# Optimization experiments

Measured on AMD Instinct MI355X. Metric: run time of the kernel, lower is better.

## Reference

```python
import jax, jax.numpy as jnp
import numpy as np

EPS = 1.1920929e-07  # torch RMSNorm default eps = finfo(float32).eps


def segsum(a):
    # a: (..., T) -> (..., T, T); [i, j] = sum_{j < t <= i} a[t] for j <= i, -inf above diag
    T = a.shape[-1]
    cs = jnp.cumsum(a, axis=-1)
    diff = cs[..., :, None] - cs[..., None, :]
    mask = jnp.tril(jnp.ones((T, T), dtype=bool))
    return jnp.where(mask, diff, -jnp.inf)


def dw_causal_conv(x, w):
    # x: (B, L, C), w: (C, K) depthwise causal conv (left pad K-1), matches Conv1d(pad=K-1)[:, :L]
    K = w.shape[-1]
    L = x.shape[1]
    xp = jnp.pad(x, ((0, 0), (K - 1, 0), (0, 0)))
    out = jnp.zeros_like(x)
    for j in range(K):
        out = out + xp[:, j:j + L, :] * w[:, j]
    return out


def ssd(X, A, Bv, Cv, block_len, init_state):
    # X: (B,L,H,P) pre-multiplied by dt; A: (B,L,H) = A*dt; Bv/Cv: (B,L,H,N)
    Bsz, L, H, P = X.shape
    N = Bv.shape[-1]
    c = L // block_len
    Xb = X.reshape(Bsz, c, block_len, H, P)
    Bb = Bv.reshape(Bsz, c, block_len, H, N)
    Cb = Cv.reshape(Bsz, c, block_len, H, N)
    Ab = A.reshape(Bsz, c, block_len, H).transpose(0, 3, 1, 2)  # (B,H,c,l)
    A_cumsum = jnp.cumsum(Ab, axis=-1)
    Ltri = jnp.exp(segsum(Ab))  # (B,H,c,l,l)
    # intra-chunk (diagonal block) output
    Y_diag = jnp.einsum('bclhn,bcshn,bhcls,bcshp->bclhp', Cb, Bb, Ltri, Xb)
    # per-chunk final states
    decay_states = jnp.exp(A_cumsum[..., -1:] - A_cumsum)  # (B,H,c,l)
    states = jnp.einsum('bclhn,bhcl,bclhp->bchpn', Bb, decay_states, Xb)
    states = jnp.concatenate([init_state[:, None], states], axis=1)  # (B,c+1,H,P,N)
    # inter-chunk recurrence via segsum over chunk boundaries
    last_A = A_cumsum[..., -1]  # (B,H,c)
    decay_chunk = jnp.exp(segsum(jnp.pad(last_A, ((0, 0), (0, 0), (1, 0)))))  # (B,H,c+1,c+1)
    new_states = jnp.einsum('bhzc,bchpn->bzhpn', decay_chunk, states)
    states, final_state = new_states[:, :-1], new_states[:, -1]
    # off-diagonal contribution from carried-in states
    state_decay_out = jnp.exp(A_cumsum)  # (B,H,c,l)
    Y_off = jnp.einsum('bclhn,bchpn,bhcl->bclhp', Cb, states, state_decay_out)
    Y = (Y_diag + Y_off).reshape(Bsz, L, H, P)
    return Y, final_state


def setup_inputs():
    key = jax.random.key(0)
    ks = jax.random.split(key, 8)
    d_model, d_state, d_conv, expand, headdim, ngroups = 1024, 128, 4, 2, 64, 1
    d_inner = expand * d_model                      # 2048
    H = d_inner // headdim                          # 32
    proj_out = 2 * d_inner + 2 * ngroups * d_state + H  # 4384
    conv_dim = d_inner + 2 * ngroups * d_state      # 2304
    B, L = 2, 2048
    x = jax.random.normal(ks[0], (B, L, d_model), dtype=jnp.float32)
    state = jnp.zeros((B, H, headdim, d_state), dtype=jnp.float32)
    in_proj_w = jax.random.normal(ks[1], (proj_out, d_model), dtype=jnp.float32) * 0.02
    conv_w = jax.random.normal(ks[2], (conv_dim, d_conv), dtype=jnp.float32) * 0.2
    A_log = jnp.log(jax.random.uniform(ks[3], (H,), minval=1.0, maxval=16.0))
    dt0 = jnp.exp(jax.random.uniform(ks[4], (H,)) * (np.log(0.1) - np.log(0.001)) + np.log(0.001))
    dt0 = jnp.maximum(dt0, 0.0001)
    dt_bias = dt0 + jnp.log(-jnp.expm1(-dt0))
    D_param = jnp.ones((H,), dtype=jnp.float32)
    norm_w = jnp.ones((d_inner,), dtype=jnp.float32)
    out_proj_w = jax.random.normal(ks[5], (d_model, d_inner), dtype=jnp.float32) * 0.02
    return dict(x=x, state=state, in_proj_w=in_proj_w, conv_w=conv_w, A_log=A_log,
                dt_bias=dt_bias, D_param=D_param, norm_w=norm_w, out_proj_w=out_proj_w,
                block_len=64)


def reference(x, state, in_proj_w, conv_w, A_log, dt_bias, D_param, norm_w, out_proj_w, block_len):
    B, L, Dm = x.shape
    H = A_log.shape[0]
    P = state.shape[2]
    N = state.shape[3]
    d_inner = H * P
    conv_dim = conv_w.shape[0]
    zxbcdt = x @ in_proj_w.T  # (B,L,proj_out)
    z = zxbcdt[..., :d_inner]
    xBC = zxbcdt[..., d_inner:d_inner + conv_dim]
    dt = zxbcdt[..., d_inner + conv_dim:]
    xBC = jax.nn.silu(dw_causal_conv(xBC, conv_w))
    x_branch = xBC[..., :d_inner]
    Bv = xBC[..., d_inner:d_inner + N]           # ngroups = 1
    Cv = xBC[..., d_inner + N:]
    X = jax.nn.silu(x_branch.reshape(B, L, H, P))
    Bv = jnp.broadcast_to(jax.nn.silu(Bv)[:, :, None, :], (B, L, H, N))
    Cv = jnp.broadcast_to(jax.nn.silu(Cv)[:, :, None, :], (B, L, H, N))
    A = -jnp.exp(A_log)
    dt = jax.nn.softplus(dt + dt_bias)           # (B,L,H)
    A_dt = A * dt
    X_dt = X * dt[..., None]
    Y, final_state = ssd(X_dt, A_dt, Bv, Cv, block_len, state)
    Y = Y + D_param[None, None, :, None] * X
    y_flat = Y.reshape(B, L, d_inner)
    y_norm = y_flat * jax.lax.rsqrt(jnp.mean(y_flat * y_flat, axis=-1, keepdims=True) + EPS) * norm_w
    y_core = y_norm * jax.nn.sigmoid(z)
    y = y_core @ out_proj_w.T + x
    return (y, final_state)
```

## Files before the change

### kernel.cpp

```cpp
#include <hip/hip_runtime.h>
#include <math.h>

#define BATCH 2
#define LSEQ  2048
#define TTOK  4096
#define DM    1024
#define DI    2048
#define NH    32
#define HP    64
#define NS    128
#define CONVD 2304
#define PROJ  4384
#define NCH   32
#define BLK   64

typedef __bf16 bf16x8 __attribute__((ext_vector_type(8)));
typedef float  f32x4  __attribute__((ext_vector_type(4)));
typedef unsigned short ushortx8 __attribute__((ext_vector_type(8)));
typedef unsigned short ushort_t;
typedef __attribute__((address_space(3))) void  lds_void;
typedef __attribute__((address_space(1))) const void glb_cvoid;

__device__ __forceinline__ float silu_(float x) { return x / (1.f + __expf(-x)); }

__device__ __forceinline__ unsigned short f2bf(float x) {
    union { float f; unsigned u; } u; u.f = x;
    unsigned r = u.u + 0x7fffu + ((u.u >> 16) & 1u);
    return (unsigned short)(r >> 16);
}
__device__ __forceinline__ float bf2f(unsigned short s) {
    union { unsigned u; float f; } u; u.u = ((unsigned)s) << 16; return u.f;
}

__global__ __launch_bounds__(256)
void cast_all_k(const float* __restrict__ x, const float* __restrict__ ipw,
                const float* __restrict__ opw,
                ushort_t* __restrict__ xb, ushort_t* __restrict__ ipb,
                ushort_t* __restrict__ opb)
{
    const int n1 = TTOK*DM, n2 = PROJ*DM;
    int i = (blockIdx.x * 256 + threadIdx.x) * 8;
    const float* src; ushort_t* dst;
    if (i < n1)            { src = x   + i;             dst = xb  + i; }
    else if (i < n1 + n2)  { src = ipw + (i - n1);      dst = ipb + (i - n1); }
    else                   { src = opw + (i - n1 - n2); dst = opb + (i - n1 - n2); }
    float4 a = *(const float4*)(src);
    float4 b = *(const float4*)(src + 4);
    ushortx8 r;
    r[0]=f2bf(a.x); r[1]=f2bf(a.y); r[2]=f2bf(a.z); r[3]=f2bf(a.w);
    r[4]=f2bf(b.x); r[5]=f2bf(b.y); r[6]=f2bf(b.z); r[7]=f2bf(b.w);
    *(ushortx8*)dst = r;
}

template<int TM, int TN, int HASRES, int OUTBF>
__global__ __launch_bounds__(256)
void hgemm_nt(const ushort_t* __restrict__ A, const ushort_t* __restrict__ Bw,
              void* __restrict__ Cp, const float* __restrict__ R,
              int M, int N, int K)
{
    constexpr int MT = TM / 32, NT = TN / 32;
    constexpr int JA = TM / 64, JB = TN / 64;
    __shared__ ushort_t S[(TM + TN) * 64];
    ushort_t* As = S;
    ushort_t* Bs = S + TM * 64;
    char* As_c = (char*)As;
    char* Bs_c = (char*)Bs;
    const int t = threadIdx.x;
    const int l = t & 63, w = t >> 6;

    const int tx_ = (N + TN - 1) / TN, ty_ = (M + TM - 1) / TM;
    int bid = blockIdx.x;
    int sc = bid / (8 * ty_), rem = bid % (8 * ty_);
    int sw_w = min(8, tx_ - sc * 8);
    int bx = sc * 8 + rem % sw_w;
    int by = rem / sw_w;
    const int bm = by * TM, bn = bx * TN;
    const int wm = (w >> 1) * (TM / 2), wn = (w & 1) * (TN / 2);

    const int rowt = t >> 2;
    const int kkt  = (t & 3) * 8;
    const ushort_t* srcA = A + (size_t)(bm + rowt) * K + kkt;
    const ushort_t* srcB[JB];
#pragma unroll
    for (int j = 0; j < JB; ++j) {
        int gr = min(bn + j * 64 + rowt, N - 1);
        srcB[j] = Bw + (size_t)gr * K + kkt;
    }

    f32x4 acc[MT][NT] = {};
    const int fr = l & 15, sel8 = (l >> 4) * 8;

    for (int k0 = 0; k0 < K; k0 += 64) {
        __syncthreads();
#pragma unroll
        for (int h = 0; h < 2; ++h) {
#pragma unroll
            for (int j = 0; j < JA; ++j)
                __builtin_amdgcn_global_load_lds((glb_cvoid*)(srcA + (size_t)j * 64 * K + k0 + h * 32),
                                                 (lds_void*)(As_c + h * TM * 64 + j * 4096 + 16 * t), 16, 0, 0);
#pragma unroll
            for (int j = 0; j < JB; ++j)
                __builtin_amdgcn_global_load_lds((glb_cvoid*)(srcB[j] + k0 + h * 32),
                                                 (lds_void*)(Bs_c + h * TN * 64 + j * 4096 + 16 * t), 16, 0, 0);
        }
        __syncthreads();
#pragma unroll
        for (int h = 0; h < 2; ++h) {
            bf16x8 af[MT], bfr[NT];
#pragma unroll
            for (int mt = 0; mt < MT; ++mt)
                af[mt] = *(const bf16x8*)(As + h * TM * 32 + (wm + mt * 16 + fr) * 32 + sel8);
#pragma unroll
            for (int nt = 0; nt < NT; ++nt)
                bfr[nt] = *(const bf16x8*)(Bs + h * TN * 32 + (wn + nt * 16 + fr) * 32 + sel8);
#pragma unroll
            for (int mt = 0; mt < MT; ++mt)
#pragma unroll
                for (int nt = 0; nt < NT; ++nt)
                    acc[mt][nt] = __builtin_amdgcn_mfma_f32_16x16x32_bf16(af[mt], bfr[nt], acc[mt][nt], 0, 0, 0);
        }
    }

    const int crow = (l >> 4) * 4, ccol = l & 15;
#pragma unroll
    for (int mt = 0; mt < MT; ++mt) {
#pragma unroll
        for (int nt = 0; nt < NT; ++nt) {
            int n = bn + wn + nt * 16 + ccol;
            if (n >= N) continue;
#pragma unroll
            for (int i = 0; i < 4; ++i) {
                int m = bm + wm + mt * 16 + crow + i;
                float v = acc[mt][nt][i];
                if (HASRES) v += R[(size_t)m * N + n];
                if (OUTBF) ((ushort_t*)Cp)[(size_t)m * N + n] = f2bf(v);
                else       ((float*)Cp)[(size_t)m * N + n] = v;
            }
        }
    }
}

#define NCONVB 9216
__global__ __launch_bounds__(256)
void mid1_k(const ushort_t* __restrict__ zx, const float* __restrict__ cw,
            const float* __restrict__ dt_bias, const float* __restrict__ A_log,
            ushort_t* __restrict__ xBC, float* __restrict__ dt_sp, float* __restrict__ cumA)
{
    if (blockIdx.x < NCONVB) {
        int idx = blockIdx.x * 256 + threadIdx.x;
        int c4 = (idx % (CONVD/4)) * 4;
        int tkk = idx / (CONVD/4);
        int b = tkk >> 11, l = tkk & 2047;
        const ushort_t* col = zx + (size_t)b * LSEQ * PROJ + DI + c4;
        float4 w0 = *(const float4*)(cw + c4*4);
        float4 w1 = *(const float4*)(cw + c4*4 + 4);
        float4 w2 = *(const float4*)(cw + c4*4 + 8);
        float4 w3 = *(const float4*)(cw + c4*4 + 12);
        ushort4 tp = *(const ushort4*)(col + (size_t)l * PROJ);
        float a0 = w0.w * bf2f(tp.x), a1 = w1.w * bf2f(tp.y), a2 = w2.w * bf2f(tp.z), a3 = w3.w * bf2f(tp.w);
        if (l >= 1) { ushort4 v = *(const ushort4*)(col + (size_t)(l-1) * PROJ);
            a0 += w0.z*bf2f(v.x); a1 += w1.z*bf2f(v.y); a2 += w2.z*bf2f(v.z); a3 += w3.z*bf2f(v.w); }
        if (l >= 2) { ushort4 v = *(const ushort4*)(col + (size_t)(l-2) * PROJ);
            a0 += w0.y*bf2f(v.x); a1 += w1.y*bf2f(v.y); a2 += w2.y*bf2f(v.z); a3 += w3.y*bf2f(v.w); }
        if (l >= 3) { ushort4 v = *(const ushort4*)(col + (size_t)(l-3) * PROJ);
            a0 += w0.x*bf2f(v.x); a1 += w1.x*bf2f(v.y); a2 += w2.x*bf2f(v.z); a3 += w3.x*bf2f(v.w); }
        ushort4 o;
        o.x = f2bf(silu_(silu_(a0))); o.y = f2bf(silu_(silu_(a1)));
        o.z = f2bf(silu_(silu_(a2))); o.w = f2bf(silu_(silu_(a3)));
        *(ushort4*)(xBC + (size_t)tkk * CONVD + c4) = o;
    } else {
        int wid = (blockIdx.x - NCONVB) * 4 + (threadIdx.x >> 6);
        int ln = threadIdx.x & 63;
        int c = wid & 31, h = (wid >> 5) & 31, b = wid >> 10;
        int tk = b * LSEQ + c * BLK + ln;
        float xv = bf2f(zx[(size_t)tk * PROJ + (DI + CONVD) + h]) + dt_bias[h];
        float dtv = (xv > 20.f) ? xv : log1pf(__expf(xv));
        dt_sp[tk * NH + h] = dtv;
        float val = -__expf(A_log[h]) * dtv;
#pragma unroll
        for (int off = 1; off < 64; off <<= 1) {
            float u = __shfl_up(val, off, 64);
            if (ln >= off) val += u;
        }
        cumA[(size_t)wid * 64 + ln] = val;
    }
}

__global__ __launch_bounds__(256)
void mid2_k(const ushort_t* __restrict__ xBC, const float* __restrict__ dt_sp,
            const float* __restrict__ cumA, float* __restrict__ CBT,
            ushort_t* __restrict__ states)
{
    __shared__ __align__(16) char smem[33408];
    int t = threadIdx.x, r = t >> 2, q = t & 3;
    if (blockIdx.x < 64) {
        int b = blockIdx.x >> 5, c = blockIdx.x & 31;
        float (*sB)[65] = (float(*)[65])smem;
        float (*sC)[65] = sB + 64;
        const ushort_t* xb = xBC + (size_t)(b * LSEQ + c * BLK) * CONVD;
        float acc[16];
#pragma unroll
        for (int i = 0; i < 16; ++i) acc[i] = 0.f;
        for (int half = 0; half < 2; ++half) {
            __syncthreads();
#pragma unroll
            for (int jj = 0; jj < 4; ++jj) {
                ushort4 bv = *(const ushort4*)(xb + (size_t)r * CONVD + DI      + half*64 + q*16 + jj*4);
                ushort4 cv = *(const ushort4*)(xb + (size_t)r * CONVD + DI + NS + half*64 + q*16 + jj*4);
                int col = q*16 + jj*4;
                sB[r][col]=bf2f(bv.x); sB[r][col+1]=bf2f(bv.y); sB[r][col+2]=bf2f(bv.z); sB[r][col+3]=bf2f(bv.w);
                sC[r][col]=bf2f(cv.x); sC[r][col+1]=bf2f(cv.y); sC[r][col+2]=bf2f(cv.z); sC[r][col+3]=bf2f(cv.w);
            }
            __syncthreads();
            for (int n = 0; n < 64; ++n) {
                float cv = sC[r][n];
#pragma unroll
                for (int si = 0; si < 16; ++si)
                    acc[si] += cv * sB[q*16 + si][n];
            }
        }
        float* o = CBT + (size_t)blockIdx.x * 4096 + r * 64 + q * 16;
#pragma unroll
        for (int si = 0; si < 16; ++si) o[si] = acc[si];
    } else {
        int bi = blockIdx.x - 64;
        int h = bi & 31, c = (bi >> 5) & 31, b = bi >> 10;
        ushort_t* XdT = (ushort_t*)smem;
        ushort_t* BdT = XdT + 64 * 72;
        const float* cA = cumA + (size_t)((b*NH + h)*NCH + c) * 64;
        float scale = dt_sp[(b * LSEQ + c * BLK + r) * NH + h] * __expf(cA[63] - cA[r]);
        const ushort_t* xb = xBC + (size_t)(b * LSEQ + c * BLK + r) * CONVD;
#pragma unroll
        for (int jj = 0; jj < 4; ++jj) {
            ushort4 v = *(const ushort4*)(xb + h*HP + q*16 + jj*4);
            int p0 = q*16 + jj*4;
            XdT[(p0+0)*72 + r] = v.x; XdT[(p0+1)*72 + r] = v.y;
            XdT[(p0+2)*72 + r] = v.z; XdT[(p0+3)*72 + r] = v.w;
        }
#pragma unroll
        for (int jj = 0; jj < 8; ++jj) {
            ushort4 v = *(const ushort4*)(xb + DI + q*32 + jj*4);
            int n0 = q*32 + jj*4;
            BdT[(n0+0)*72 + r] = f2bf(bf2f(v.x)*scale);
            BdT[(n0+1)*72 + r] = f2bf(bf2f(v.y)*scale);
            BdT[(n0+2)*72 + r] = f2bf(bf2f(v.z)*scale);
            BdT[(n0+3)*72 + r] = f2bf(bf2f(v.w)*scale);
        }
        __syncthreads();
        int ln = t & 63, w = t >> 6;
        int wm = (w >> 1) * 32, wn = (w & 1) * 64;
        int fr = ln & 15;
        f32x4 acc[2][4] = {};
#pragma unroll
        for (int ks = 0; ks < 2; ++ks) {
            int koff = ks*32 + (ln >> 4) * 8;
            bf16x8 af[2], bv[4];
#pragma unroll
            for (int mt = 0; mt < 2; ++mt) af[mt] = *(const bf16x8*)&XdT[(wm + mt*16 + fr)*72 + koff];
#pragma unroll
            for (int nt = 0; nt < 4; ++nt) bv[nt] = *(const bf16x8*)&BdT[(wn + nt*16 + fr)*72 + koff];
#pragma unroll
            for (int mt = 0; mt < 2; ++mt)
#pragma unroll
                for (int nt = 0; nt < 4; ++nt)
                    acc[mt][nt] = __builtin_amdgcn_mfma_f32_16x16x32_bf16(af[mt], bv[nt], acc[mt][nt], 0, 0, 0);
        }
        ushort_t* o = states + (size_t)((b*NCH + c)*NH + h) * 8192;
        int crow = (ln >> 4) * 4, ccol = ln & 15;
#pragma unroll
        for (int mt = 0; mt < 2; ++mt)
#pragma unroll
            for (int nt = 0; nt < 4; ++nt)
#pragma unroll
                for (int i = 0; i < 4; ++i)
                    o[(wm + mt*16 + crow + i)*128 + wn + nt*16 + ccol] = f2bf(acc[mt][nt][i]);
    }
}

__global__ __launch_bounds__(256)
void scan_k(const float* __restrict__ init_state, const float* __restrict__ cumA,
            const ushort_t* __restrict__ states, ushort_t* __restrict__ pref,
            float* __restrict__ out_final)
{
    int idx = blockIdx.x * 256 + threadIdx.x;
    int h = (idx >> 13) & 31, b = idx >> 18;
    int pn = idx & 8191;
    float run = init_state[idx];
    const float* cAb = cumA + (size_t)(b*NH + h) * NCH * 64;
    for (int c = 0; c < NCH; ++c) {
        float la = cAb[c*64 + 63];
        size_t off = (size_t)((b*NCH + c)*NH + h) * 8192 + pn;
        float tmp = bf2f(states[off]);
        pref[off] = f2bf(run);
        run = expf(la) * run + tmp;
    }
    out_final[idx] = run;
}

__global__ __launch_bounds__(256)
void y_mfma_k(const ushort_t* __restrict__ xBC, const float* __restrict__ dt_sp,
              const float* __restrict__ cumA, const float* __restrict__ CBT,
              const ushort_t* __restrict__ pref, const float* __restrict__ D_param,
              ushort_t* __restrict__ Y)
{
    int bi = blockIdx.x;
    int h = bi & 31, c = (bi >> 5) & 31, b = bi >> 10;
    __shared__ ushort_t Wm[64 * 72];
    __shared__ ushort_t XT[64 * 72];
    __shared__ ushort_t Cd[64 * 136];
    __shared__ ushort_t Sp[64 * 136];
    __shared__ float sCA[64];
    __shared__ float sdt[64];
    int t = threadIdx.x, r = t >> 2, q = t & 3;
    const float* cA = cumA + (size_t)((b*NH + h)*NCH + c) * 64;
    if (t < 64) {
        sCA[t] = cA[t];
        sdt[t] = dt_sp[(b * LSEQ + c * BLK + t) * NH + h];
    }
    __syncthreads();
    size_t row = (size_t)(b * LSEQ + c * BLK + r);
    const ushort_t* xb = xBC + row * CONVD;
    float myA = sCA[r], eC = __expf(myA);
    const float* cbt = CBT + (size_t)(b*NCH + c) * 4096 + r * 64;
#pragma unroll
    for (int j = 0; j < 16; ++j) {
        int s = q*16 + j;
        float wv = (s <= r) ? cbt[s] * __expf(myA - sCA[s]) * sdt[s] : 0.f;
        Wm[r*72 + s] = f2bf(wv);
    }
#pragma unroll
    for (int jj = 0; jj < 4; ++jj) {
        ushort4 v = *(const ushort4*)(xb + h*HP + q*16 + jj*4);
        int p0 = q*16 + jj*4;
        XT[(p0+0)*72 + r] = v.x; XT[(p0+1)*72 + r] = v.y;
        XT[(p0+2)*72 + r] = v.z; XT[(p0+3)*72 + r] = v.w;
    }
#pragma unroll
    for (int jj = 0; jj < 8; ++jj) {
        ushort4 v = *(const ushort4*)(xb + DI + NS + q*32 + jj*4);
        int n0 = q*32 + jj*4;
        Cd[r*136 + n0+0] = f2bf(bf2f(v.x)*eC);
        Cd[r*136 + n0+1] = f2bf(bf2f(v.y)*eC);
        Cd[r*136 + n0+2] = f2bf(bf2f(v.z)*eC);
        Cd[r*136 + n0+3] = f2bf(bf2f(v.w)*eC);
    }
    const ushort_t* pr = pref + (size_t)((b*NCH + c)*NH + h) * 8192 + r * 128;
#pragma unroll
    for (int jj = 0; jj < 4; ++jj) {
        ushortx8 v = *(const ushortx8*)(pr + q*32 + jj*8);
        *(ushortx8*)&Sp[r*136 + q*32 + jj*8] = v;
    }
    __syncthreads();
    int ln = t & 63, w = t >> 6;
    int wm = (w >> 1) * 32, wn = (w & 1) * 32;
    int fr = ln & 15;
    f32x4 acc[2][2] = {};
#pragma unroll
    for (int ks = 0; ks < 2; ++ks) {
        int koff = ks*32 + (ln >> 4) * 8;
        bf16x8 af[2], bv[2];
#pragma unroll
        for (int mt = 0; mt < 2; ++mt) af[mt] = *(const bf16x8*)&Wm[(wm + mt*16 + fr)*72 + koff];
#pragma unroll
        for (int nt = 0; nt < 2; ++nt) bv[nt] = *(const bf16x8*)&XT[(wn + nt*16 + fr)*72 + koff];
#pragma unroll
        for (int mt = 0; mt < 2; ++mt)
#pragma unroll
            for (int nt = 0; nt < 2; ++nt)
                acc[mt][nt] = __builtin_amdgcn_mfma_f32_16x16x32_bf16(af[mt], bv[nt], acc[mt][nt], 0, 0, 0);
    }
#pragma unroll
    for (int ks = 0; ks < 4; ++ks) {
        int koff = ks*32 + (ln >> 4) * 8;
        bf16x8 af[2], bv[2];
#pragma unroll
        for (int mt = 0; mt < 2; ++mt) af[mt] = *(const bf16x8*)&Cd[(wm + mt*16 + fr)*136 + koff];
#pragma unroll
        for (int nt = 0; nt < 2; ++nt) bv[nt] = *(const bf16x8*)&Sp[(wn + nt*16 + fr)*136 + koff];
#pragma unroll
        for (int mt = 0; mt < 2; ++mt)
#pragma unroll
            for (int nt = 0; nt < 2; ++nt)
                acc[mt][nt] = __builtin_amdgcn_mfma_f32_16x16x32_bf16(af[mt], bv[nt], acc[mt][nt], 0, 0, 0);
    }
    float Dh = D_param[h];
    int crow = (ln >> 4) * 4, ccol = ln & 15;
#pragma unroll
    for (int mt = 0; mt < 2; ++mt)
#pragma unroll
        for (int nt = 0; nt < 2; ++nt)
#pragma unroll
            for (int i = 0; i < 4; ++i) {
                int li = wm + mt*16 + crow + i;
                int p  = wn + nt*16 + ccol;
                size_t rr = (size_t)(b*LSEQ + c*BLK + li);
                float xv = bf2f(xBC[rr * CONVD + h*HP + p]);
                Y[rr * DI + h*HP + p] = f2bf(acc[mt][nt][i] + Dh * xv);
            }
}

__global__ __launch_bounds__(256)
void rms_gate_k(const ushort_t* __restrict__ zx, const float* __restrict__ norm_w,
                const ushort_t* __restrict__ Y, ushort_t* __restrict__ Yb)
{
    int tk = blockIdx.x, t = threadIdx.x;
    const ushort_t* rowp = Y + (size_t)tk * DI + t*8;
    ushortx8 v = *(const ushortx8*)rowp;
    float f[8];
    float ss = 0.f;
#pragma unroll
    for (int i = 0; i < 8; ++i) { f[i] = bf2f(v[i]); ss += f[i]*f[i]; }
#pragma unroll
    for (int off = 32; off > 0; off >>= 1) ss += __shfl_xor(ss, off, 64);
    __shared__ float sw[4];
    __shared__ float stot;
    if ((t & 63) == 0) sw[t >> 6] = ss;
    __syncthreads();
    if (t == 0) stot = rsqrtf((sw[0]+sw[1]+sw[2]+sw[3]) * (1.f/DI) + 1.1920929e-07f);
    __syncthreads();
    float scale = stot;
    const ushort_t* zr = zx + (size_t)tk * PROJ + t*8;
    ushortx8 z = *(const ushortx8*)zr;
    float4 w0 = *(const float4*)(norm_w + t*8);
    float4 w1 = *(const float4*)(norm_w + t*8 + 4);
    float wv[8] = {w0.x,w0.y,w0.z,w0.w,w1.x,w1.y,w1.z,w1.w};
    ushortx8 o;
#pragma unroll
    for (int i = 0; i < 8; ++i)
        o[i] = f2bf(f[i]*scale*wv[i] / (1.f+__expf(-bf2f(z[i]))));
    *(ushortx8*)(Yb + (size_t)tk * DI + t*8) = o;
}

extern "C" void kernel_launch(void* const* d_in, const int* in_sizes, int n_in,
                              void* d_out, int out_size, void* d_ws, size_t ws_size,
                              hipStream_t stream)
{
    const float* x        = (const float*)d_in[0];
    const float* init_st  = (const float*)d_in[1];
    const float* in_proj  = (const float*)d_in[2];
    const float* conv_w   = (const float*)d_in[3];
    const float* A_log    = (const float*)d_in[4];
    const float* dt_bias  = (const float*)d_in[5];
    const float* D_param  = (const float*)d_in[6];
    const float* norm_w   = (const float*)d_in[7];
    const float* out_proj = (const float*)d_in[8];
    float* out = (float*)d_out;

    ushort_t* zx_bf  = (ushort_t*)d_ws;
    ushort_t* xBC_bf = zx_bf + (size_t)TTOK*PROJ;
    float* dt_sp  = (float*)(xBC_bf + (size_t)TTOK*CONVD);
    float* cumA   = dt_sp  + (size_t)TTOK*NH;
    float* CBTb   = cumA   + (size_t)TTOK*NH;
    ushort_t* states = (ushort_t*)(CBTb + 262144);
    ushort_t* pref = states + 16777216;
    float* Yreg   = (float*)(pref + 16777216);
    ushort_t* opw_bf = (ushort_t*)(Yreg + (size_t)TTOK*DI);
    ushort_t* Y_bf   = (ushort_t*)Yreg;
    ushort_t* xb_bf  = (ushort_t*)Yreg;
    ushort_t* ipw_bf = xb_bf + (size_t)TTOK*DM;
    ushort_t* Yb_bf  = xBC_bf;

    const int nc = (TTOK*DM + PROJ*DM + DM*DI) / (256*8);
    cast_all_k<<<nc, 256, 0, stream>>>(x, in_proj, out_proj, xb_bf, ipw_bf, opw_bf);
    hgemm_nt<128,128,0,1><<<((PROJ+127)/128)*(TTOK/128), 256, 0, stream>>>(xb_bf, ipw_bf, zx_bf, nullptr, TTOK, PROJ, DM);
    mid1_k<<<NCONVB + BATCH*NH*NCH/4, 256, 0, stream>>>(zx_bf, conv_w, dt_bias, A_log, xBC_bf, dt_sp, cumA);
    mid2_k<<<64 + BATCH*NCH*NH, 256, 0, stream>>>(xBC_bf, dt_sp, cumA, CBTb, states);
    scan_k<<<(BATCH*NH*HP*NS)/256, 256, 0, stream>>>(init_st, cumA, states, pref, out + (size_t)TTOK*DM);
    y_mfma_k<<<BATCH*NCH*NH, 256, 0, stream>>>(xBC_bf, dt_sp, cumA, CBTb, pref, D_param, Y_bf);
    rms_gate_k<<<TTOK, 256, 0, stream>>>(zx_bf, norm_w, Y_bf, Yb_bf);
    hgemm_nt<128,64,1,0><<<(DM/64)*(TTOK/128), 256, 0, stream>>>(Yb_bf, opw_bf, out, x, TTOK, DM, DI);
}
```

Measured before the change: 297.7 us.

## Halve GEMM K-tile, vectorize scan by four, reuse LDS X for D term

```diff
diff --git a/kernel.cpp b/kernel.cpp
--- a/kernel.cpp
+++ b/kernel.cpp
@@ -60,9 +60,9 @@
 {
     constexpr int MT = TM / 32, NT = TN / 32;
     constexpr int JA = TM / 64, JB = TN / 64;
-    __shared__ ushort_t S[(TM + TN) * 64];
+    __shared__ ushort_t S[(TM + TN) * 32];
     ushort_t* As = S;
-    ushort_t* Bs = S + TM * 64;
+    ushort_t* Bs = S + TM * 32;
     char* As_c = (char*)As;
     char* Bs_c = (char*)Bs;
     const int t = threadIdx.x;
@@ -90,35 +90,29 @@
     f32x4 acc[MT][NT] = {};
     const int fr = l & 15, sel8 = (l >> 4) * 8;
 
-    for (int k0 = 0; k0 < K; k0 += 64) {
+    for (int k0 = 0; k0 < K; k0 += 32) {
         __syncthreads();
 #pragma unroll
-        for (int h = 0; h < 2; ++h) {
-#pragma unroll
-            for (int j = 0; j < JA; ++j)
-                __builtin_amdgcn_global_load_lds((glb_cvoid*)(srcA + (size_t)j * 64 * K + k0 + h * 32),
-                                                 (lds_void*)(As_c + h * TM * 64 + j * 4096 + 16 * t), 16, 0, 0);
-#pragma unroll
-            for (int j = 0; j < JB; ++j)
-                __builtin_amdgcn_global_load_lds((glb_cvoid*)(srcB[j] + k0 + h * 32),
-                                                 (lds_void*)(Bs_c + h * TN * 64 + j * 4096 + 16 * t), 16, 0, 0);
-        }
+        for (int j = 0; j < JA; ++j)
+            __builtin_amdgcn_global_load_lds((glb_cvoid*)(srcA + (size_t)j * 64 * K + k0),
+                                             (lds_void*)(As_c + j * 4096 + 16 * t), 16, 0, 0);
+#pragma unroll
+        for (int j = 0; j < JB; ++j)
+            __builtin_amdgcn_global_load_lds((glb_cvoid*)(srcB[j] + k0),
+                                             (lds_void*)(Bs_c + j * 4096 + 16 * t), 16, 0, 0);
         __syncthreads();
-#pragma unroll
-        for (int h = 0; h < 2; ++h) {
-            bf16x8 af[MT], bfr[NT];
-#pragma unroll
-            for (int mt = 0; mt < MT; ++mt)
-                af[mt] = *(const bf16x8*)(As + h * TM * 32 + (wm + mt * 16 + fr) * 32 + sel8);
+        bf16x8 af[MT], bfr[NT];
+#pragma unroll
+        for (int mt = 0; mt < MT; ++mt)
+            af[mt] = *(const bf16x8*)(As + (wm + mt * 16 + fr) * 32 + sel8);
+#pragma unroll
+        for (int nt = 0; nt < NT; ++nt)
+            bfr[nt] = *(const bf16x8*)(Bs + (wn + nt * 16 + fr) * 32 + sel8);
+#pragma unroll
+        for (int mt = 0; mt < MT; ++mt)
 #pragma unroll
             for (int nt = 0; nt < NT; ++nt)
-                bfr[nt] = *(const bf16x8*)(Bs + h * TN * 32 + (wn + nt * 16 + fr) * 32 + sel8);
-#pragma unroll
-            for (int mt = 0; mt < MT; ++mt)
-#pragma unroll
-                for (int nt = 0; nt < NT; ++nt)
-                    acc[mt][nt] = __builtin_amdgcn_mfma_f32_16x16x32_bf16(af[mt], bfr[nt], acc[mt][nt], 0, 0, 0);
-        }
+                acc[mt][nt] = __builtin_amdgcn_mfma_f32_16x16x32_bf16(af[mt], bfr[nt], acc[mt][nt], 0, 0, 0);
     }
 
     const int crow = (l >> 4) * 4, ccol = l & 15;
@@ -282,19 +276,24 @@
             const ushort_t* __restrict__ states, ushort_t* __restrict__ pref,
             float* __restrict__ out_final)
 {
-    int idx = blockIdx.x * 256 + threadIdx.x;
+    int idx = (blockIdx.x * 256 + threadIdx.x) * 4;
     int h = (idx >> 13) & 31, b = idx >> 18;
     int pn = idx & 8191;
-    float run = init_state[idx];
+    float4 run = *(const float4*)(init_state + idx);
     const float* cAb = cumA + (size_t)(b*NH + h) * NCH * 64;
     for (int c = 0; c < NCH; ++c) {
-        float la = cAb[c*64 + 63];
+        float e = expf(cAb[c*64 + 63]);
         size_t off = (size_t)((b*NCH + c)*NH + h) * 8192 + pn;
-        float tmp = bf2f(states[off]);
-        pref[off] = f2bf(run);
-        run = expf(la) * run + tmp;
-    }
-    out_final[idx] = run;
+        ushort4 s = *(const ushort4*)(states + off);
+        ushort4 p;
+        p.x = f2bf(run.x); p.y = f2bf(run.y); p.z = f2bf(run.z); p.w = f2bf(run.w);
+        *(ushort4*)(pref + off) = p;
+        run.x = e * run.x + bf2f(s.x);
+        run.y = e * run.y + bf2f(s.y);
+        run.z = e * run.z + bf2f(s.z);
+        run.w = e * run.w + bf2f(s.w);
+    }
+    *(float4*)(out_final + idx) = run;
 }
 
 __global__ __launch_bounds__(256)
@@ -394,7 +393,7 @@
                 int li = wm + mt*16 + crow + i;
                 int p  = wn + nt*16 + ccol;
                 size_t rr = (size_t)(b*LSEQ + c*BLK + li);
-                float xv = bf2f(xBC[rr * CONVD + h*HP + p]);
+                float xv = bf2f(XT[p*72 + li]);
                 Y[rr * DI + h*HP + p] = f2bf(acc[mt][nt][i] + Dh * xv);
             }
 }
@@ -465,7 +464,7 @@
     hgemm_nt<128,128,0,1><<<((PROJ+127)/128)*(TTOK/128), 256, 0, stream>>>(xb_bf, ipw_bf, zx_bf, nullptr, TTOK, PROJ, DM);
     mid1_k<<<NCONVB + BATCH*NH*NCH/4, 256, 0, stream>>>(zx_bf, conv_w, dt_bias, A_log, xBC_bf, dt_sp, cumA);
     mid2_k<<<64 + BATCH*NCH*NH, 256, 0, stream>>>(xBC_bf, dt_sp, cumA, CBTb, states);
-    scan_k<<<(BATCH*NH*HP*NS)/256, 256, 0, stream>>>(init_st, cumA, states, pref, out + (size_t)TTOK*DM);
+    scan_k<<<(BATCH*NH*HP*NS)/(256*4), 256, 0, stream>>>(init_st, cumA, states, pref, out + (size_t)TTOK*DM);
     y_mfma_k<<<BATCH*NCH*NH, 256, 0, stream>>>(xBC_bf, dt_sp, cumA, CBTb, pref, D_param, Y_bf);
     rms_gate_k<<<TTOK, 256, 0, stream>>>(zx_bf, norm_w, Y_bf, Yb_bf);
     hgemm_nt<128,64,1,0><<<(DM/64)*(TTOK/128), 256, 0, stream>>>(Yb_bf, opw_bf, out, x, TTOK, DM, DI);
```

New measurement: 309.6 us. 4.0% more time.
